# Performance work log

Measured on AMD Instinct MI355X. Metric: run time of the kernel, lower is better.

Reference implementation:

```python
import jax, jax.numpy as jnp
import numpy as np

B, S, L = 64, 512, 768


def setup_inputs() -> dict:
    key = jax.random.key(0)
    k1, k2 = jax.random.split(key)
    x = jax.random.normal(k1, (B, S, L), dtype=jnp.float32)
    # matches torch uniform_(-0.1, 0.1) init for the probe matrix b
    b = jax.random.uniform(k2, (L, L), minval=-0.1, maxval=0.1, dtype=jnp.float32)
    return {"x": x, "b": b}


def reference(x, b):
    # Original: z[b,i,j,h] = x_i - x_j; h = einsum('gh,bijh', b, z); dist = sum_g h^2
    # Identity: ||b @ (x_i - x_j)||^2 = ||p_i||^2 + ||p_j||^2 - 2 p_i . p_j,  p = x @ b^T
    p = jnp.einsum('gh,bsh->bsg', b, x)          # [B, S, L] projected points
    sq = jnp.sum(p * p, axis=-1)                 # [B, S]  squared norms
    gram = jnp.einsum('bsg,btg->bst', p, p)      # [B, S, S] inner products
    return sq[:, :, None] + sq[:, None, :] - 2.0 * gram  # [B, S, S]
```

## Files before the change

### kernel.cpp

```cpp
#include <hip/hip_runtime.h>
#include <hip/hip_bf16.h>


using bf16x8 = __attribute__((ext_vector_type(8))) __bf16;
using f32x4  = __attribute__((ext_vector_type(4))) float;
using fl4    = __attribute__((ext_vector_type(4))) float;
using u16x4  = __attribute__((ext_vector_type(4))) unsigned short;

#define NB 64
#define NS 512
#define NL 768
#define NM (NB * NS)

__device__ __forceinline__ unsigned short f2bf(float f) {
  unsigned u = __builtin_bit_cast(unsigned, f);
  u += 0x7FFFu + ((u >> 16) & 1u);
  return (unsigned short)(u >> 16);
}

__device__ __forceinline__ void gload_lds16(const void* g, void* l) {
  __builtin_amdgcn_global_load_lds(
      (const __attribute__((address_space(1))) void*)g,
      (__attribute__((address_space(3))) void*)l, 16, 0, 0);
}

__global__ __launch_bounds__(256) void k_cvt_b(const float* __restrict__ b,
                                               unsigned short* __restrict__ bb) {
  const long t = (long)blockIdx.x * 256 + threadIdx.x;
  fl4 v = *(const fl4*)(b + t * 4);
  u16x4 o;
#pragma unroll
  for (int j = 0; j < 4; ++j) o[j] = f2bf(v[j]);
  *(u16x4*)(bb + t * 4) = o;
}

__global__ __launch_bounds__(256) void k_proj(const float* __restrict__ x,
                                              const unsigned short* __restrict__ bb,
                                              unsigned short* __restrict__ p) {
  __shared__ unsigned short smA[128 * 32];
  __shared__ unsigned short smB[128 * 32];
  const int tid = threadIdx.x;
  const int w = tid >> 6, l = tid & 63;
  const int wg = ((blockIdx.x & 7) * 192) + (blockIdx.x >> 3);
  const int nt = wg % 6, mt = wg / 6;
  const long m0 = (long)mt * 128, n0 = (long)nt * 128;
  const int wr = (w >> 1) * 64, wc = (w & 1) * 64;

  const int arow = tid >> 3;
  const int akk  = (tid & 7) * 4;
  const float* gA = x + (m0 + arow) * NL + akk;
  const int brow = tid >> 2;
  const int bkq  = (tid & 3) * 8;
  const unsigned short* gB = bb + (n0 + brow) * (long)NL + bkq;
  char* ldsB0 = (char*)smB + w * 1024;

  const int qh = l >> 4, lr = l & 15;
  const int aoff = (wr + lr) * 64 + qh * 16;
  const int boff = (wc + lr) * 64 + qh * 16;

  f32x4 acc[4][4] = {};
#pragma unroll 1
  for (int kt = 0; kt < 24; ++kt) {
    const int k0 = kt * 32;
    __syncthreads();
    gload_lds16(gB + k0, ldsB0);
    gload_lds16(gB + k0 + 64 * NL, ldsB0 + 4096);
    fl4 va0 = *(const fl4*)(gA + k0);
    fl4 va1 = *(const fl4*)(gA + k0 + 32 * NL);
    fl4 va2 = *(const fl4*)(gA + k0 + 64 * NL);
    fl4 va3 = *(const fl4*)(gA + k0 + 96 * NL);
    u16x4 o0, o1, o2, o3;
#pragma unroll
    for (int j = 0; j < 4; ++j) {
      o0[j] = f2bf(va0[j]); o1[j] = f2bf(va1[j]);
      o2[j] = f2bf(va2[j]); o3[j] = f2bf(va3[j]);
    }
    *(u16x4*)((char*)smA + 0 * 2048 + tid * 8) = o0;
    *(u16x4*)((char*)smA + 1 * 2048 + tid * 8) = o1;
    *(u16x4*)((char*)smA + 2 * 2048 + tid * 8) = o2;
    *(u16x4*)((char*)smA + 3 * 2048 + tid * 8) = o3;
    __syncthreads();
    bf16x8 fa[4], fb[4];
#pragma unroll
    for (int m = 0; m < 4; ++m)
      fa[m] = *(const bf16x8*)((const char*)smA + aoff + m * 1024);
#pragma unroll
    for (int n = 0; n < 4; ++n)
      fb[n] = *(const bf16x8*)((const char*)smB + boff + n * 1024);
#pragma unroll
    for (int m = 0; m < 4; ++m)
#pragma unroll
      for (int n = 0; n < 4; ++n)
        acc[m][n] = __builtin_amdgcn_mfma_f32_16x16x32_bf16(fa[m], fb[n], acc[m][n], 0, 0, 0);
  }
#pragma unroll
  for (int m = 0; m < 4; ++m) {
    const long rbase = m0 + wr + m * 16 + qh * 4;
#pragma unroll
    for (int n = 0; n < 4; ++n) {
      const long col = n0 + wc + n * 16 + lr;
#pragma unroll
      for (int r = 0; r < 4; ++r)
        p[(rbase + r) * NL + col] = f2bf(acc[m][n][r]);
    }
  }
}

__global__ __launch_bounds__(256) void k_sq(const unsigned short* __restrict__ p,
                                            float* __restrict__ sq) {
  const int row = blockIdx.x * 4 + (threadIdx.x >> 6);
  const int l = threadIdx.x & 63;
  const unsigned short* pr = p + (long)row * NL;
  float s = 0.f;
#pragma unroll
  for (int c = 0; c < 3; ++c) {
    u16x4 v = *(const u16x4*)(pr + (c * 64 + l) * 4);
#pragma unroll
    for (int j = 0; j < 4; ++j) {
      float f = __builtin_bit_cast(float, ((unsigned)v[j]) << 16);
      s += f * f;
    }
  }
#pragma unroll
  for (int d = 32; d >= 1; d >>= 1) s += __shfl_xor(s, d, 64);
  if (l == 0) sq[row] = s;
}

__global__ __launch_bounds__(256) void k_gram(const unsigned short* __restrict__ p,
                                              const float* __restrict__ sq,
                                              float* __restrict__ out) {
  __shared__ unsigned short smA[128 * 32];
  __shared__ unsigned short smB[128 * 32];
  const int tid = threadIdx.x;
  const int w = tid >> 6, l = tid & 63;
  const int wg = ((blockIdx.x & 7) * 128) + (blockIdx.x >> 3);
  const int batch = wg >> 4, tile = wg & 15;
  const int mt = tile >> 2, nt = tile & 3;
  const unsigned short* pb = p + (long)batch * NS * NL;
  const long m0 = (long)mt * 128, n0 = (long)nt * 128;
  const int wr = (w >> 1) * 64, wc = (w & 1) * 64;

  const int srow = tid >> 2;
  const int skq  = (tid & 3) * 8;
  const unsigned short* gA = pb + (m0 + srow) * (long)NL + skq;
  const unsigned short* gB = pb + (n0 + srow) * (long)NL + skq;
  char* ldsA0 = (char*)smA + w * 1024;
  char* ldsB0 = (char*)smB + w * 1024;

  const int qh = l >> 4, lr = l & 15;
  const int aoff = (wr + lr) * 64 + qh * 16;
  const int boff = (wc + lr) * 64 + qh * 16;

  f32x4 acc[4][4] = {};
#pragma unroll 1
  for (int kt = 0; kt < 24; ++kt) {
    const int k0 = kt * 32;
    __syncthreads();
    gload_lds16(gA + k0, ldsA0);
    gload_lds16(gA + k0 + 64 * NL, ldsA0 + 4096);
    gload_lds16(gB + k0, ldsB0);
    gload_lds16(gB + k0 + 64 * NL, ldsB0 + 4096);
    __syncthreads();
    bf16x8 fa[4], fb[4];
#pragma unroll
    for (int m = 0; m < 4; ++m)
      fa[m] = *(const bf16x8*)((const char*)smA + aoff + m * 1024);
#pragma unroll
    for (int n = 0; n < 4; ++n)
      fb[n] = *(const bf16x8*)((const char*)smB + boff + n * 1024);
#pragma unroll
    for (int m = 0; m < 4; ++m)
#pragma unroll
      for (int n = 0; n < 4; ++n)
        acc[m][n] = __builtin_amdgcn_mfma_f32_16x16x32_bf16(fa[m], fb[n], acc[m][n], 0, 0, 0);
  }
  const float* sqb = sq + batch * NS;
  float* outb = out + (long)batch * NS * NS;
  float sqc[4];
#pragma unroll
  for (int n = 0; n < 4; ++n) sqc[n] = sqb[n0 + wc + n * 16 + lr];
#pragma unroll
  for (int m = 0; m < 4; ++m) {
#pragma unroll
    for (int r = 0; r < 4; ++r) {
      const long row = m0 + wr + m * 16 + qh * 4 + r;
      const float sr = sqb[row];
#pragma unroll
      for (int n = 0; n < 4; ++n) {
        const long col = n0 + wc + n * 16 + lr;
        outb[row * NS + col] = sr + sqc[n] - 2.0f * acc[m][n][r];
      }
    }
  }
}

extern "C" void kernel_launch(void* const* d_in, const int* in_sizes, int n_in,
                              void* d_out, int out_size, void* d_ws, size_t ws_size,
                              hipStream_t stream) {
  (void)in_sizes; (void)n_in; (void)out_size; (void)ws_size;
  const float* x = (const float*)d_in[0];
  const float* b = (const float*)d_in[1];
  float* out = (float*)d_out;
  char* ws = (char*)d_ws;
  unsigned short* bb = (unsigned short*)ws;
  float* sq          = (float*)(ws + 1179648);
  unsigned short* p  = (unsigned short*)(ws + 1310720);

  k_cvt_b<<<576, 256, 0, stream>>>(b, bb);
  k_proj <<<1536, 256, 0, stream>>>(x, bb, p);
  k_sq   <<<8192, 256, 0, stream>>>(p, sq);
  k_gram <<<1024, 256, 0, stream>>>(p, sq, out);
}
```

Baseline: 123.1 us.

## Double-buffer LDS in proj and gram GEMMs with swizzled layout and direct fp32 staging

Both GEMM kernels now use two LDS buffers so the global-to-LDS load for the next K tile is issued before computing on the current one, removing one barrier per iteration. The projection kernel stages fp32 x directly into LDS via global_load_lds and converts to bf16 at fragment-load time with v_cvt_pk_bf16_f32, instead of converting in registers before storing. Column XOR swizzles are applied to the LDS layouts to reduce bank conflicts. The cost is doubled LDS (more for fp32 A), which may reduce occupancy, and the correctness of the swizzle pattern depends on the async loads and the reads agreeing on layout.

```diff
diff --git a/kernel.cpp b/kernel.cpp
--- a/kernel.cpp
+++ b/kernel.cpp
@@ -6,11 +6,11 @@
 using f32x4  = __attribute__((ext_vector_type(4))) float;
 using fl4    = __attribute__((ext_vector_type(4))) float;
 using u16x4  = __attribute__((ext_vector_type(4))) unsigned short;
+using u32x4  = __attribute__((ext_vector_type(4))) unsigned int;
 
 #define NB 64
 #define NS 512
 #define NL 768
-#define NM (NB * NS)
 
 __device__ __forceinline__ unsigned short f2bf(float f) {
   unsigned u = __builtin_bit_cast(unsigned, f);
@@ -22,6 +22,16 @@
   __builtin_amdgcn_global_load_lds(
       (const __attribute__((address_space(1))) void*)g,
       (__attribute__((address_space(3))) void*)l, 16, 0, 0);
+}
+
+__device__ __forceinline__ bf16x8 cvt_bf8(fl4 a, fl4 b) {
+  unsigned r0, r1, r2, r3;
+  asm("v_cvt_pk_bf16_f32 %0, %1, %2" : "=v"(r0) : "v"(a[0]), "v"(a[1]));
+  asm("v_cvt_pk_bf16_f32 %0, %1, %2" : "=v"(r1) : "v"(a[2]), "v"(a[3]));
+  asm("v_cvt_pk_bf16_f32 %0, %1, %2" : "=v"(r2) : "v"(b[0]), "v"(b[1]));
+  asm("v_cvt_pk_bf16_f32 %0, %1, %2" : "=v"(r3) : "v"(b[2]), "v"(b[3]));
+  u32x4 t = {r0, r1, r2, r3};
+  return __builtin_bit_cast(bf16x8, t);
 }
 
 __global__ __launch_bounds__(256) void k_cvt_b(const float* __restrict__ b,
@@ -37,8 +47,8 @@
 __global__ __launch_bounds__(256) void k_proj(const float* __restrict__ x,
                                               const unsigned short* __restrict__ bb,
                                               unsigned short* __restrict__ p) {
-  __shared__ unsigned short smA[128 * 32];
-  __shared__ unsigned short smB[128 * 32];
+  __shared__ __align__(16) float          smA[2][128 * 32];
+  __shared__ __align__(16) unsigned short smB[2][128 * 32];
   const int tid = threadIdx.x;
   const int w = tid >> 6, l = tid & 63;
   const int wg = ((blockIdx.x & 7) * 192) + (blockIdx.x >> 3);
@@ -47,52 +57,69 @@
   const int wr = (w >> 1) * 64, wc = (w & 1) * 64;
 
   const int arow = tid >> 3;
-  const int akk  = (tid & 7) * 4;
-  const float* gA = x + (m0 + arow) * NL + akk;
+  const int acol = ((tid & 7) ^ (arow & 7)) * 4;
+  const float* gA = x + (m0 + arow) * (long)NL + acol;
   const int brow = tid >> 2;
-  const int bkq  = (tid & 3) * 8;
-  const unsigned short* gB = bb + (n0 + brow) * (long)NL + bkq;
-  char* ldsB0 = (char*)smB + w * 1024;
+  const int bcol = ((tid & 3) ^ (brow & 3)) * 8;
+  const unsigned short* gB = bb + (n0 + brow) * (long)NL + bcol;
 
   const int qh = l >> 4, lr = l & 15;
-  const int aoff = (wr + lr) * 64 + qh * 16;
-  const int boff = (wc + lr) * 64 + qh * 16;
+  const int aoff = (wr + lr) * 128;
+  const int asw1 = (qh * 32) ^ ((lr & 7) << 4);
+  const int asw2 = (qh * 32 + 16) ^ ((lr & 7) << 4);
+  const int boff = (wc + lr) * 64 + ((qh ^ (lr & 3)) << 4);
 
   f32x4 acc[4][4] = {};
+
+#define STAGE_A(k0, buf)                                                     \
+  {                                                                          \
+    char* d_ = (char*)&smA[buf][0] + w * 1024;                               \
+    const float* s_ = gA + (k0);                                             \
+    gload_lds16(s_ + 0 * 32 * NL, d_ + 0 * 4096);                            \
+    gload_lds16(s_ + 1 * 32 * NL, d_ + 1 * 4096);                            \
+    gload_lds16(s_ + 2 * 32 * NL, d_ + 2 * 4096);                            \
+    gload_lds16(s_ + 3 * 32 * NL, d_ + 3 * 4096);                            \
+  }
+#define STAGE_B(k0, buf)                                                     \
+  {                                                                          \
+    char* d_ = (char*)&smB[buf][0] + w * 1024;                               \
+    const unsigned short* s_ = gB + (k0);                                    \
+    gload_lds16(s_, d_);                                                     \
+    gload_lds16(s_ + 64 * NL, d_ + 4096);                                    \
+  }
+
+  STAGE_A(0, 0)
+  STAGE_B(0, 0)
+  __syncthreads();
+  int cur = 0;
 #pragma unroll 1
   for (int kt = 0; kt < 24; ++kt) {
-    const int k0 = kt * 32;
-    __syncthreads();
-    gload_lds16(gB + k0, ldsB0);
-    gload_lds16(gB + k0 + 64 * NL, ldsB0 + 4096);
-    fl4 va0 = *(const fl4*)(gA + k0);
-    fl4 va1 = *(const fl4*)(gA + k0 + 32 * NL);
-    fl4 va2 = *(const fl4*)(gA + k0 + 64 * NL);
-    fl4 va3 = *(const fl4*)(gA + k0 + 96 * NL);
-    u16x4 o0, o1, o2, o3;
-#pragma unroll
-    for (int j = 0; j < 4; ++j) {
-      o0[j] = f2bf(va0[j]); o1[j] = f2bf(va1[j]);
-      o2[j] = f2bf(va2[j]); o3[j] = f2bf(va3[j]);
-    }
-    *(u16x4*)((char*)smA + 0 * 2048 + tid * 8) = o0;
-    *(u16x4*)((char*)smA + 1 * 2048 + tid * 8) = o1;
-    *(u16x4*)((char*)smA + 2 * 2048 + tid * 8) = o2;
-    *(u16x4*)((char*)smA + 3 * 2048 + tid * 8) = o3;
-    __syncthreads();
+    if (kt < 23) {
+      STAGE_A((kt + 1) * 32, cur ^ 1)
+      STAGE_B((kt + 1) * 32, cur ^ 1)
+    }
+    const char* A  = (const char*)&smA[cur][0];
+    const char* Bb = (const char*)&smB[cur][0];
     bf16x8 fa[4], fb[4];
 #pragma unroll
-    for (int m = 0; m < 4; ++m)
-      fa[m] = *(const bf16x8*)((const char*)smA + aoff + m * 1024);
+    for (int m = 0; m < 4; ++m) {
+      fl4 a0 = *(const fl4*)(A + aoff + m * 2048 + asw1);
+      fl4 a1 = *(const fl4*)(A + aoff + m * 2048 + asw2);
+      fa[m] = cvt_bf8(a0, a1);
+    }
 #pragma unroll
     for (int n = 0; n < 4; ++n)
-      fb[n] = *(const bf16x8*)((const char*)smB + boff + n * 1024);
+      fb[n] = *(const bf16x8*)(Bb + boff + n * 1024);
 #pragma unroll
     for (int m = 0; m < 4; ++m)
 #pragma unroll
       for (int n = 0; n < 4; ++n)
         acc[m][n] = __builtin_amdgcn_mfma_f32_16x16x32_bf16(fa[m], fb[n], acc[m][n], 0, 0, 0);
-  }
+    __syncthreads();
+    cur ^= 1;
+  }
+#undef STAGE_A
+#undef STAGE_B
 #pragma unroll
   for (int m = 0; m < 4; ++m) {
     const long rbase = m0 + wr + m * 16 + qh * 4;
@@ -129,8 +156,8 @@
 __global__ __launch_bounds__(256) void k_gram(const unsigned short* __restrict__ p,
                                               const float* __restrict__ sq,
                                               float* __restrict__ out) {
-  __shared__ unsigned short smA[128 * 32];
-  __shared__ unsigned short smB[128 * 32];
+  __shared__ __align__(16) unsigned short smA[2][128 * 32];
+  __shared__ __align__(16) unsigned short smB[2][128 * 32];
   const int tid = threadIdx.x;
   const int w = tid >> 6, l = tid & 63;
   const int wg = ((blockIdx.x & 7) * 128) + (blockIdx.x >> 3);
@@ -141,39 +168,50 @@
   const int wr = (w >> 1) * 64, wc = (w & 1) * 64;
 
   const int srow = tid >> 2;
-  const int skq  = (tid & 3) * 8;
-  const unsigned short* gA = pb + (m0 + srow) * (long)NL + skq;
-  const unsigned short* gB = pb + (n0 + srow) * (long)NL + skq;
-  char* ldsA0 = (char*)smA + w * 1024;
-  char* ldsB0 = (char*)smB + w * 1024;
+  const int scol = ((tid & 3) ^ (srow & 3)) * 8;
+  const unsigned short* gA = pb + (m0 + srow) * (long)NL + scol;
+  const unsigned short* gB = pb + (n0 + srow) * (long)NL + scol;
 
   const int qh = l >> 4, lr = l & 15;
-  const int aoff = (wr + lr) * 64 + qh * 16;
-  const int boff = (wc + lr) * 64 + qh * 16;
+  const int aoff = (wr + lr) * 64 + ((qh ^ (lr & 3)) << 4);
+  const int boff = (wc + lr) * 64 + ((qh ^ (lr & 3)) << 4);
 
   f32x4 acc[4][4] = {};
+
+#define STAGE2(k0, buf)                                                      \
+  {                                                                          \
+    char* da_ = (char*)&smA[buf][0] + w * 1024;                              \
+    char* db_ = (char*)&smB[buf][0] + w * 1024;                              \
+    gload_lds16(gA + (k0), da_);                                             \
+    gload_lds16(gA + (k0) + 64 * NL, da_ + 4096);                            \
+    gload_lds16(gB + (k0), db_);                                             \
+    gload_lds16(gB + (k0) + 64 * NL, db_ + 4096);                            \
+  }
+
+  STAGE2(0, 0)
+  __syncthreads();
+  int cur = 0;
 #pragma unroll 1
   for (int kt = 0; kt < 24; ++kt) {
-    const int k0 = kt * 32;
-    __syncthreads();
-    gload_lds16(gA + k0, ldsA0);
-    gload_lds16(gA + k0 + 64 * NL, ldsA0 + 4096);
-    gload_lds16(gB + k0, ldsB0);
-    gload_lds16(gB + k0 + 64 * NL, ldsB0 + 4096);
-    __syncthreads();
+    if (kt < 23) STAGE2((kt + 1) * 32, cur ^ 1)
+    const char* A  = (const char*)&smA[cur][0];
+    const char* Bb = (const char*)&smB[cur][0];
     bf16x8 fa[4], fb[4];
 #pragma unroll
     for (int m = 0; m < 4; ++m)
-      fa[m] = *(const bf16x8*)((const char*)smA + aoff + m * 1024);
+      fa[m] = *(const bf16x8*)(A + aoff + m * 1024);
 #pragma unroll
     for (int n = 0; n < 4; ++n)
-      fb[n] = *(const bf16x8*)((const char*)smB + boff + n * 1024);
+      fb[n] = *(const bf16x8*)(Bb + boff + n * 1024);
 #pragma unroll
     for (int m = 0; m < 4; ++m)
 #pragma unroll
       for (int n = 0; n < 4; ++n)
         acc[m][n] = __builtin_amdgcn_mfma_f32_16x16x32_bf16(fa[m], fb[n], acc[m][n], 0, 0, 0);
-  }
+    __syncthreads();
+    cur ^= 1;
+  }
+#undef STAGE2
   const float* sqb = sq + batch * NS;
   float* outb = out + (long)batch * NS * NS;
   float sqc[4];
```

New measurement: 118.7 us. 1.04x faster.
